# Kernel optimization log

Hardware: AMD Instinct MI355X
Metric: run time of the kernel (lower is better)

Reference implementation:

```python
import jax, jax.numpy as jnp
import numpy as np

B, S, D, H, HD = 1, 4096, 1024, 16, 64
HALF = HD // 2


def setup_inputs() -> dict:
    key = jax.random.key(0)
    ks = jax.random.split(key, 8)
    std = 0.02
    x = jax.random.normal(ks[0], (B, S, D), dtype=jnp.float32)
    wq_w = jax.random.normal(ks[1], (D, D), dtype=jnp.float32) * std
    wk_w = jax.random.normal(ks[2], (D, D), dtype=jnp.float32) * std
    wv_w = jax.random.normal(ks[3], (D, D), dtype=jnp.float32) * std
    wo_w = jax.random.normal(ks[4], (D, D), dtype=jnp.float32) * std
    wq_b = jnp.zeros((D,), jnp.float32)
    wk_b = jnp.zeros((D,), jnp.float32)
    wv_b = jnp.zeros((D,), jnp.float32)
    wo_b = jnp.zeros((D,), jnp.float32)
    # LLaMA-style rotary frequencies: theta = 10000^{-2i/HD}
    inv_freq = 1.0 / (10000.0 ** (jnp.arange(0, HD, 2, dtype=jnp.float32) / HD))  # [HALF]
    t = jnp.arange(S, dtype=jnp.float32)
    angles = jnp.outer(t, inv_freq)  # [S, HALF]
    freqs_cos = jnp.cos(angles)
    freqs_sin = jnp.sin(angles)
    # causal additive mask (finite large-negative to stay grad-safe)
    mask = jnp.triu(jnp.full((S, S), -1e9, dtype=jnp.float32), k=1)[None, None]
    return {
        "x": x, "start_pos": 0, "freqs_cos": freqs_cos, "freqs_sin": freqs_sin,
        "mask": mask,
        "wq_w": wq_w, "wq_b": wq_b, "wk_w": wk_w, "wk_b": wk_b,
        "wv_w": wv_w, "wv_b": wv_b, "wo_w": wo_w, "wo_b": wo_b,
    }


def _apply_rope(t, cos, sin):
    # t: [B, S, H, HD]; cos/sin: [S, HALF]. Complex multiply on consecutive pairs.
    b, s, h, hd = t.shape
    t2 = t.reshape(b, s, h, hd // 2, 2)
    x0, x1 = t2[..., 0], t2[..., 1]
    c = cos[None, :, None, :]
    sn = sin[None, :, None, :]
    o0 = x0 * c - x1 * sn
    o1 = x0 * sn + x1 * c
    return jnp.stack([o0, o1], axis=-1).reshape(b, s, h, hd)


def reference(x, start_pos, freqs_cos, freqs_sin, mask,
              wq_w, wq_b, wk_w, wk_b, wv_w, wv_b, wo_w, wo_b):
    bsz, seqlen, dim = x.shape
    q = (x @ wq_w.T + wq_b).reshape(bsz, seqlen, H, HD)
    k = (x @ wk_w.T + wk_b).reshape(bsz, seqlen, H, HD)
    v = (x @ wv_w.T + wv_b).reshape(bsz, seqlen, H, HD)
    q = _apply_rope(q, freqs_cos, freqs_sin)
    k = _apply_rope(k, freqs_cos, freqs_sin)
    # [B, H, S, HD]
    q = q.transpose(0, 2, 1, 3)
    k = k.transpose(0, 2, 1, 3)
    v = v.transpose(0, 2, 1, 3)
    scores = jnp.einsum('bhqd,bhkd->bhqk', q, k) / jnp.sqrt(jnp.float32(HD))
    scores = scores + mask
    probs = jax.nn.softmax(scores.astype(jnp.float32), axis=-1).astype(q.dtype)
    out = jnp.einsum('bhqk,bhkd->bhqd', probs, v)  # [B, H, S, HD]
    out = out.transpose(0, 2, 1, 3).reshape(bsz, seqlen, dim)
    return out @ wo_w.T + wo_b
```

## Files before the change

kernel.cpp:

```cpp
#include <hip/hip_runtime.h>


#define S_LEN 4096
#define DIM   1024
#define NH    16
#define HD    64

typedef __attribute__((ext_vector_type(8))) short bf16x8;
typedef __attribute__((ext_vector_type(4))) float f32x4;

__device__ __forceinline__ unsigned short f2b(float f) {
  union { float f; unsigned int u; } v; v.f = f;
  unsigned int r = (v.u + 0x7fffu + ((v.u >> 16) & 1u)) >> 16;
  return (unsigned short)r;
}
__device__ __forceinline__ float b2f(unsigned short h) {
  union { unsigned int u; float f; } v; v.u = ((unsigned int)h) << 16;
  return v.f;
}
__device__ __forceinline__ unsigned int pk2t(float a, float b) {
  union { float f; unsigned int u; } x, y; x.f = a; y.f = b;
  return (x.u >> 16) | (y.u & 0xffff0000u);
}
__device__ __forceinline__ void gload16(const void* g, void* l) {
  __builtin_amdgcn_global_load_lds(
      (const __attribute__((address_space(1))) unsigned int*)g,
      (__attribute__((address_space(3))) unsigned int*)l, 16, 0, 0);
}
__device__ __forceinline__ f32x4 fzero4() { f32x4 z = {0.f, 0.f, 0.f, 0.f}; return z; }

__device__ __forceinline__ bf16x8 lds_swz(const unsigned short* s, int row, int chunk) {
  int byte = row * 128 + ((chunk ^ (row & 7)) << 4);
  return *(const bf16x8*)((const char*)s + byte);
}

__global__ void cvt_all(const float* __restrict__ x, const float* __restrict__ wq,
                        const float* __restrict__ wk, const float* __restrict__ wv,
                        const float* __restrict__ wo, const float* __restrict__ qb,
                        const float* __restrict__ kb, const float* __restrict__ vbs,
                        const float* __restrict__ ob, unsigned short* __restrict__ xb,
                        unsigned short* __restrict__ wqkvb, unsigned short* __restrict__ wobb,
                        float* __restrict__ biasq, float* __restrict__ biaso) {
  int i = blockIdx.x * 256 + threadIdx.x;
  if (i < 2097152) {
    const float* src; unsigned short* dst; int off;
    if (i < 1048576)      { src = x;  dst = xb;              off = i; }
    else if (i < 1310720) { src = wq; dst = wqkvb;           off = i - 1048576; }
    else if (i < 1572864) { src = wk; dst = wqkvb + 1048576; off = i - 1310720; }
    else if (i < 1835008) { src = wv; dst = wqkvb + 2097152; off = i - 1572864; }
    else                  { src = wo; dst = wobb;            off = i - 1835008; }
    float4 v = ((const float4*)src)[off];
    unsigned int lo = (unsigned int)f2b(v.x) | ((unsigned int)f2b(v.y) << 16);
    unsigned int hi = (unsigned int)f2b(v.z) | ((unsigned int)f2b(v.w) << 16);
    ((uint2*)dst)[off] = make_uint2(lo, hi);
  } else if (i < 2097152 + 1024) {
    int j = i - 2097152;
    if (j < 256)      ((float4*)biasq)[j]              = ((const float4*)qb)[j];
    else if (j < 512) ((float4*)(biasq + 1024))[j-256] = ((const float4*)kb)[j-256];
    else if (j < 768) ((float4*)(biasq + 2048))[j-512] = ((const float4*)vbs)[j-512];
    else              ((float4*)biaso)[j-768]          = ((const float4*)ob)[j-768];
  }
}

__global__ __launch_bounds__(512, 2) void gemm_qkv(
    const unsigned short* __restrict__ A, const unsigned short* __restrict__ B,
    const float* __restrict__ bias, unsigned short* __restrict__ dq,
    unsigned short* __restrict__ dk, unsigned short* __restrict__ vtout,
    const float* __restrict__ fc, const float* __restrict__ fs, int K) {
  __shared__ alignas(16) unsigned short sA[2][256 * 64];
  __shared__ alignas(16) unsigned short sB[2][256 * 64];
  const int tid = threadIdx.x;
  const int lane = tid & 63, wave = tid >> 6;
  const int ln = lane & 15, quad = lane >> 4;
  const int bm = blockIdx.x * 256, bn = blockIdx.y * 256;
  const int wr = (wave >> 2) * 128, wc = (wave & 3) * 64;
  const int NT = K >> 6;

  f32x4 acc[8][4];
#pragma unroll
  for (int i = 0; i < 8; ++i)
#pragma unroll
    for (int j = 0; j < 4; ++j) acc[i][j] = fzero4();

#define STAGE(tt, ch) do {                                                   \
    int o_ = ((ch) * 512 + tid) * 8;                                         \
    int row_ = o_ >> 6, c_ = (o_ >> 3) & 7;                                  \
    int col_ = ((tt) << 6) + ((c_ ^ (row_ & 7)) << 3);                       \
    int bs_ = (tt) & 1;                                                      \
    gload16(A + (size_t)(bm + row_) * K + col_, (char*)sA[bs_] + o_ * 2);    \
    gload16(B + (size_t)(bn + row_) * K + col_, (char*)sB[bs_] + o_ * 2);    \
  } while (0)
#define BAR()   __builtin_amdgcn_s_barrier()
#define LGKM0() asm volatile("s_waitcnt lgkmcnt(0)" ::: "memory")

  STAGE(0, 0); STAGE(0, 1); STAGE(0, 2); STAGE(0, 3); STAGE(1, 0);
  asm volatile("s_waitcnt vmcnt(2)" ::: "memory");
  BAR();

#pragma unroll 2
  for (int t = 0; t < 16; ++t) {
    const unsigned short* cA = sA[t & 1];
    const unsigned short* cB = sB[t & 1];
    bf16x8 a0[4], a1[4], b0[4], b1[4];

#pragma unroll
    for (int j = 0; j < 4; ++j) b0[j] = lds_swz(cB, wc + j * 16 + ln, quad);
#pragma unroll
    for (int i = 0; i < 4; ++i) a0[i] = lds_swz(cA, wr + i * 16 + ln, quad);
    if (t + 1 < NT) STAGE(t + 1, 1);
    BAR(); LGKM0();
    __builtin_amdgcn_s_setprio(1);
#pragma unroll
    for (int i = 0; i < 4; ++i)
#pragma unroll
      for (int j = 0; j < 4; ++j)
        acc[i][j] = __builtin_amdgcn_mfma_f32_16x16x32_bf16(a0[i], b0[j], acc[i][j], 0, 0, 0);
    __builtin_amdgcn_s_setprio(0);
    BAR();

#pragma unroll
    for (int i = 0; i < 4; ++i) a1[i] = lds_swz(cA, wr + (i + 4) * 16 + ln, quad);
#pragma unroll
    for (int j = 0; j < 4; ++j) b1[j] = lds_swz(cB, wc + j * 16 + ln, 4 + quad);
    if (t + 1 < NT) STAGE(t + 1, 2);
    BAR(); LGKM0();
    __builtin_amdgcn_s_setprio(1);
#pragma unroll
    for (int i = 0; i < 4; ++i)
#pragma unroll
      for (int j = 0; j < 4; ++j)
        acc[i + 4][j] = __builtin_amdgcn_mfma_f32_16x16x32_bf16(a1[i], b0[j], acc[i + 4][j], 0, 0, 0);
    __builtin_amdgcn_s_setprio(0);
    BAR();

#pragma unroll
    for (int i = 0; i < 4; ++i) a0[i] = lds_swz(cA, wr + i * 16 + ln, 4 + quad);
#pragma unroll
    for (int i = 0; i < 4; ++i) a1[i] = lds_swz(cA, wr + (i + 4) * 16 + ln, 4 + quad);
    if (t + 1 < NT) STAGE(t + 1, 3);
    BAR(); LGKM0();
    __builtin_amdgcn_s_setprio(1);
#pragma unroll
    for (int i = 0; i < 4; ++i)
#pragma unroll
      for (int j = 0; j < 4; ++j)
        acc[i][j] = __builtin_amdgcn_mfma_f32_16x16x32_bf16(a0[i], b1[j], acc[i][j], 0, 0, 0);
    __builtin_amdgcn_s_setprio(0);
    BAR();

    if (t + 2 < NT) STAGE(t + 2, 0);
    BAR(); LGKM0();
    __builtin_amdgcn_s_setprio(1);
#pragma unroll
    for (int i = 0; i < 4; ++i)
#pragma unroll
      for (int j = 0; j < 4; ++j)
        acc[i + 4][j] = __builtin_amdgcn_mfma_f32_16x16x32_bf16(a1[i], b1[j], acc[i + 4][j], 0, 0, 0);
    __builtin_amdgcn_s_setprio(0);
    if (t < 14) {
      asm volatile("s_waitcnt vmcnt(2)" ::: "memory");
      BAR();
    } else if (t == 14) {
      asm volatile("s_waitcnt vmcnt(0)" ::: "memory");
      BAR();
    }
  }
#undef STAGE
#undef BAR
#undef LGKM0

  const int bufi = bn >> 10;
  const int hq = ((bn & 1023) + wc) >> 6;
  if (bufi < 2) {
    unsigned short* const base = bufi == 0 ? dq : dk;
    const float qsc = bufi == 0 ? 0.180336880f : 1.0f;
#pragma unroll
    for (int i = 0; i < 8; ++i)
#pragma unroll
      for (int j = 0; j < 4; ++j) {
        int n = bn + wc + j * 16 + ln;
        float bi = bias[n];
        int hd = j * 16 + ln;
        int pi = hd >> 1;
        bool evn = (ln & 1) == 0;
#pragma unroll
        for (int r = 0; r < 4; ++r) {
          int m = bm + wr + i * 16 + quad * 4 + r;
          float val = acc[i][j][r] + bi;
          float par = __shfl_xor(val, 1);
          float c = fc[m * 32 + pi], sn = fs[m * 32 + pi];
          float o = evn ? (val * c - par * sn) : (par * sn + val * c);
          base[((size_t)(hq * S_LEN + m)) * HD + hd] = f2b(o * qsc);
        }
      }
  } else {
    __syncthreads();
    unsigned short* scr =
        (wave < 4 ? (unsigned short*)sA : (unsigned short*)sB) + (wave & 3) * 8192;
#pragma unroll
    for (int i = 0; i < 8; ++i)
#pragma unroll
      for (int j = 0; j < 4; ++j) {
        int n = bn + wc + j * 16 + ln;
        float bi = bias[n];
        int hd = j * 16 + ln;
#pragma unroll
        for (int r = 0; r < 4; ++r) {
          int sl = i * 16 + quad * 4 + r;
          int byte = hd * 256 + ((((sl >> 3) ^ (hd & 7)) << 4)) + (sl & 7) * 2;
          *(unsigned short*)((char*)scr + byte) = f2b(acc[i][j][r] + bi);
        }
      }
    __syncthreads();
#pragma unroll
    for (int pass = 0; pass < 4; ++pass) {
      int row = pass * 16 + ln;
      uint4 d[4];
#pragma unroll
      for (int j = 0; j < 4; ++j) {
        int c = quad * 4 + j;
        d[j] = *(uint4*)((char*)scr + row * 256 + ((c ^ (row & 7)) << 4));
      }
      uint4* dst = (uint4*)(vtout + ((size_t)(hq * HD + row)) * S_LEN + bm + wr + quad * 32);
#pragma unroll
      for (int j = 0; j < 4; ++j) dst[j] = d[j];
    }
  }
}

__global__ __launch_bounds__(256) void gemm_out(
    const unsigned short* __restrict__ A, const unsigned short* __restrict__ B,
    const float* __restrict__ bias, float* __restrict__ outF, int N, int K) {
  __shared__ alignas(16) unsigned short sA[2][128 * 32];
  __shared__ alignas(16) unsigned short sB[2][64 * 32];
  const int tid = threadIdx.x;
  const int lane = tid & 63, wave = tid >> 6;
  const int ln = lane & 15, quad = lane >> 4;
  const int bm = blockIdx.x * 128, bn = blockIdx.y * 64;
  const int wr = (wave >> 1) * 64, wc = (wave & 1) * 32;

  f32x4 acc[4][2];
#pragma unroll
  for (int i = 0; i < 4; ++i)
#pragma unroll
    for (int j = 0; j < 2; ++j) acc[i][j] = fzero4();

  {
#pragma unroll
    for (int i = 0; i < 2; ++i) {
      int o = (i * 256 + tid) * 16;
      int e = o >> 1;
      int row = e >> 5, col = e & 31;
      gload16(A + (size_t)(bm + row) * K + col, (char*)sA[0] + o);
    }
    int o = tid * 16;
    int e = o >> 1;
    int row = e >> 5, col = e & 31;
    gload16(B + (size_t)(bn + row) * K + col, (char*)sB[0] + o);
  }

  int buf = 0;
  for (int k0 = 0; k0 < K; k0 += 32, buf ^= 1) {
    __syncthreads();
    if (k0 + 32 < K) {
#pragma unroll
      for (int i = 0; i < 2; ++i) {
        int o = (i * 256 + tid) * 16;
        int e = o >> 1;
        int row = e >> 5, col = e & 31;
        gload16(A + (size_t)(bm + row) * K + k0 + 32 + col, (char*)sA[buf ^ 1] + o);
      }
      int o = tid * 16;
      int e = o >> 1;
      int row = e >> 5, col = e & 31;
      gload16(B + (size_t)(bn + row) * K + k0 + 32 + col, (char*)sB[buf ^ 1] + o);
    }
    bf16x8 af[4], bfr[2];
#pragma unroll
    for (int i = 0; i < 4; ++i)
      af[i] = *(const bf16x8*)&sA[buf][(wr + i * 16 + ln) * 32 + quad * 8];
#pragma unroll
    for (int j = 0; j < 2; ++j)
      bfr[j] = *(const bf16x8*)&sB[buf][(wc + j * 16 + ln) * 32 + quad * 8];
#pragma unroll
    for (int i = 0; i < 4; ++i)
#pragma unroll
      for (int j = 0; j < 2; ++j)
        acc[i][j] = __builtin_amdgcn_mfma_f32_16x16x32_bf16(af[i], bfr[j], acc[i][j], 0, 0, 0);
  }

#pragma unroll
  for (int i = 0; i < 4; ++i)
#pragma unroll
    for (int j = 0; j < 2; ++j) {
      int n = bn + wc + j * 16 + ln;
      float bi = bias[n];
#pragma unroll
      for (int r = 0; r < 4; ++r) {
        int m = bm + wr + i * 16 + quad * 4 + r;
        outF[(size_t)m * N + n] = acc[i][j][r] + bi;
      }
    }
}

__global__ __launch_bounds__(512, 4) void flash_kernel(
    const unsigned short* __restrict__ qg, const unsigned short* __restrict__ kg,
    const unsigned short* __restrict__ vtg, unsigned short* __restrict__ attn) {
  __shared__ alignas(16) unsigned short sK[2][2][64 * 64];
  __shared__ alignas(16) unsigned short sV[2][2][64 * 64];

  const int tid = threadIdx.x;
  const int lane = tid & 63, wave = tid >> 6;
  const int w = wave & 3, grp = wave >> 2;
  const int ln = lane & 15, quad = lane >> 4;
  const int c = blockIdx.x;
  const int h = c & 15;
  const int qt = 63 - (c >> 4);
  const int qrow = qt * 64 + w * 16;

  const unsigned short* qh = qg + (size_t)h * (S_LEN * HD);
  const unsigned short* kh = kg + (size_t)h * (S_LEN * HD);
  const unsigned short* vh = vtg + (size_t)h * (HD * S_LEN);

  bf16x8 qf[2];
  qf[0] = *(const bf16x8*)(qh + (size_t)(qrow + ln) * HD + quad * 8);
  qf[1] = *(const bf16x8*)(qh + (size_t)(qrow + ln) * HD + 32 + quad * 8);

  f32x4 o_acc[4];
  f32x4 l_acc = fzero4();
#pragma unroll
  for (int t = 0; t < 4; ++t) o_acc[t] = fzero4();
  bf16x8 ones;
#pragma unroll
  for (int j = 0; j < 8; ++j) ones[j] = (short)0x3F80;

  const int nst = (qt + 2) >> 1;
  const int srow = tid >> 3, sch = tid & 7;
  const int kswz = (sch ^ (srow & 7)) << 3;

  gload16(kh + (size_t)srow * HD + kswz, (char*)sK[0][0] + tid * 16);
  gload16(kh + (size_t)(64 + srow) * HD + kswz, (char*)sK[0][1] + tid * 16);
  gload16(vh + (size_t)srow * S_LEN + kswz, (char*)sV[0][0] + tid * 16);
  gload16(vh + (size_t)srow * S_LEN + 64 + kswz, (char*)sV[0][1] + tid * 16);

  const unsigned short* kEp = kh + (size_t)(128 + srow) * HD + kswz;
  const unsigned short* kOp = kEp + (size_t)64 * HD;
  const unsigned short* vEp = vh + (size_t)srow * S_LEN + 128 + kswz;
  const unsigned short* vOp = vEp + 64;

  int buf = 0;
  for (int s = 0; s < nst; ++s, buf ^= 1) {
    __syncthreads();
    if (s + 1 < nst) {
      gload16(kEp, (char*)sK[buf ^ 1][0] + tid * 16);
      gload16(kOp, (char*)sK[buf ^ 1][1] + tid * 16);
      gload16(vEp, (char*)sV[buf ^ 1][0] + tid * 16);
      gload16(vOp, (char*)sV[buf ^ 1][1] + tid * 16);
      kEp += (size_t)128 * HD; kOp += (size_t)128 * HD;
      vEp += 128; vOp += 128;
    }
    const int kt = 2 * s + grp;
    if (kt > qt) continue;
    const unsigned short* kp = sK[buf][grp];
    const unsigned short* vp = sV[buf][grp];

    f32x4 sc[4];
#pragma unroll
    for (int t = 0; t < 4; ++t) sc[t] = fzero4();
    __builtin_amdgcn_s_setprio(1);
#pragma unroll
    for (int t = 0; t < 4; ++t) {
      bf16x8 kb0 = lds_swz(kp, t * 16 + ln, quad);
      bf16x8 kb1 = lds_swz(kp, t * 16 + ln, 4 + quad);
      sc[t] = __builtin_amdgcn_mfma_f32_16x16x32_bf16(kb0, qf[0], sc[t], 0, 0, 0);
      sc[t] = __builtin_amdgcn_mfma_f32_16x16x32_bf16(kb1, qf[1], sc[t], 0, 0, 0);
    }
    __builtin_amdgcn_s_setprio(0);

    float e[4][4];
    if (kt == qt) {
#pragma unroll
      for (int t = 0; t < 4; ++t)
#pragma unroll
        for (int r = 0; r < 4; ++r) {
          int kvl = 16 * t + quad * 4 + r;
          e[t][r] = (kvl <= w * 16 + ln) ? __builtin_amdgcn_exp2f(sc[t][r]) : 0.0f;
        }
    } else {
#pragma unroll
      for (int t = 0; t < 4; ++t)
#pragma unroll
        for (int r = 0; r < 4; ++r) e[t][r] = __builtin_amdgcn_exp2f(sc[t][r]);
    }

    unsigned int x0 = pk2t(e[0][0], e[0][1]), x1 = pk2t(e[0][2], e[0][3]);
    unsigned int y0 = pk2t(e[1][0], e[1][1]), y1 = pk2t(e[1][2], e[1][3]);
    unsigned int z0 = pk2t(e[2][0], e[2][1]), z1 = pk2t(e[2][2], e[2][3]);
    unsigned int w0 = pk2t(e[3][0], e[3][1]), w1 = pk2t(e[3][2], e[3][3]);
    auto a32 = __builtin_amdgcn_permlane32_swap(x0, y0, false, false);
    auto a16 = __builtin_amdgcn_permlane16_swap(a32[0], a32[1], false, false);
    auto b32 = __builtin_amdgcn_permlane32_swap(x1, y1, false, false);
    auto b16 = __builtin_amdgcn_permlane16_swap(b32[0], b32[1], false, false);
    auto c32 = __builtin_amdgcn_permlane32_swap(z0, w0, false, false);
    auto c16 = __builtin_amdgcn_permlane16_swap(c32[0], c32[1], false, false);
    auto d32 = __builtin_amdgcn_permlane32_swap(z1, w1, false, false);
    auto d16 = __builtin_amdgcn_permlane16_swap(d32[0], d32[1], false, false);
    union { uint4 u; bf16x8 b; } pa0u, pa1u;
    pa0u.u = make_uint4(a16[0], b16[0], a16[1], b16[1]);
    pa1u.u = make_uint4(c16[0], d16[0], c16[1], d16[1]);
    const bf16x8 pa0 = pa0u.b, pa1 = pa1u.b;

    __builtin_amdgcn_s_setprio(1);
    l_acc = __builtin_amdgcn_mfma_f32_16x16x32_bf16(pa0, ones, l_acc, 0, 0, 0);
    l_acc = __builtin_amdgcn_mfma_f32_16x16x32_bf16(pa1, ones, l_acc, 0, 0, 0);
#pragma unroll
    for (int t = 0; t < 4; ++t) {
      bf16x8 vb0 = lds_swz(vp, t * 16 + ln, quad);
      bf16x8 vb1 = lds_swz(vp, t * 16 + ln, 4 + quad);
      o_acc[t] = __builtin_amdgcn_mfma_f32_16x16x32_bf16(pa0, vb0, o_acc[t], 0, 0, 0);
      o_acc[t] = __builtin_amdgcn_mfma_f32_16x16x32_bf16(pa1, vb1, o_acc[t], 0, 0, 0);
    }
    __builtin_amdgcn_s_setprio(0);
  }

  __syncthreads();
  float* mrg = (float*)sK;
  const int mi = (w * 64 + lane) * 20;
  if (grp == 1) {
    *(f32x4*)&mrg[mi +  0] = o_acc[0];
    *(f32x4*)&mrg[mi +  4] = o_acc[1];
    *(f32x4*)&mrg[mi +  8] = o_acc[2];
    *(f32x4*)&mrg[mi + 12] = o_acc[3];
    *(f32x4*)&mrg[mi + 16] = l_acc;
  }
  __syncthreads();
  if (grp == 0) {
    o_acc[0] += *(const f32x4*)&mrg[mi + 0];
    o_acc[1] += *(const f32x4*)&mrg[mi + 4];
    o_acc[2] += *(const f32x4*)&mrg[mi + 8];
    o_acc[3] += *(const f32x4*)&mrg[mi + 12];
    l_acc += *(const f32x4*)&mrg[mi + 16];
    float inv[4];
#pragma unroll
    for (int r = 0; r < 4; ++r) inv[r] = 1.0f / l_acc[r];
#pragma unroll
    for (int t = 0; t < 4; ++t)
#pragma unroll
      for (int r = 0; r < 4; ++r) {
        int row = qrow + quad * 4 + r;
        attn[(size_t)row * DIM + h * HD + t * 16 + ln] = f2b(o_acc[t][r] * inv[r]);
      }
  }
}

extern "C" void kernel_launch(void* const* d_in, const int* in_sizes, int n_in,
                              void* d_out, int out_size, void* d_ws, size_t ws_size,
                              hipStream_t stream) {
  const float* x    = (const float*)d_in[0];
  const float* fc   = (const float*)d_in[2];
  const float* fs   = (const float*)d_in[3];
  const float* wqw  = (const float*)d_in[5];
  const float* wqb  = (const float*)d_in[6];
  const float* wkw  = (const float*)d_in[7];
  const float* wkb  = (const float*)d_in[8];
  const float* wvw  = (const float*)d_in[9];
  const float* wvb  = (const float*)d_in[10];
  const float* wow  = (const float*)d_in[11];
  const float* wobf = (const float*)d_in[12];
  float* out = (float*)d_out;

  char* ws = (char*)d_ws;
  const size_t MB = (size_t)1 << 20;
  unsigned short* xb    = (unsigned short*)(ws + 0);
  unsigned short* wqkvb = (unsigned short*)(ws + 8 * MB);
  unsigned short* wobb  = (unsigned short*)(ws + 16 * MB);
  float* biasq = (float*)(ws + 18 * MB);
  float* biaso = (float*)(ws + 18 * MB + 65536);
  unsigned short* qb_ = (unsigned short*)(ws + 19 * MB);
  unsigned short* kb_ = (unsigned short*)(ws + 27 * MB);
  unsigned short* vt  = (unsigned short*)(ws + 35 * MB);
  unsigned short* attn = (unsigned short*)(ws + 0);

  cvt_all<<<8196, 256, 0, stream>>>(x, wqw, wkw, wvw, wow, wqb, wkb, wvb, wobf,
                                    xb, wqkvb, wobb, biasq, biaso);
  gemm_qkv<<<dim3(16, 12), 512, 0, stream>>>(xb, wqkvb, biasq, qb_, kb_, vt, fc, fs, 1024);
  flash_kernel<<<1024, 512, 0, stream>>>(qb_, kb_, vt, attn);
  gemm_out<<<dim3(32, 16), 256, 0, stream>>>(attn, wobb, biaso, out, 1024, 1024);
}
```

Before: 247.7 us.

## Process 128-row query tiles per block so K/V tiles are reused twice

Each wave now handles 32 query rows (two 16-row fragments) instead of 16, so every block covers 128 query rows and the grid is halved. Each K and V fragment read from LDS feeds two MFMA chains, which halves LDS traffic and K/V global loads per query row. The query-tile order is also remapped to interleave long and short causal tiles for load balance. In exchange, each wave holds more registers, fewer blocks run, and the merge step uses both the K and V shared buffers.

```diff
diff --git a/kernel.cpp b/kernel.cpp
--- a/kernel.cpp
+++ b/kernel.cpp
@@ -315,26 +315,30 @@
   const int ln = lane & 15, quad = lane >> 4;
   const int c = blockIdx.x;
   const int h = c & 15;
-  const int qt = 63 - (c >> 4);
-  const int qrow = qt * 64 + w * 16;
+  const int k5 = c >> 4;
+  const int P = (k5 < 16) ? (31 - k5) : (k5 - 16);
+  const int qrow = P * 128 + w * 32;
+  const int nst = P + 1;
 
   const unsigned short* qh = qg + (size_t)h * (S_LEN * HD);
   const unsigned short* kh = kg + (size_t)h * (S_LEN * HD);
   const unsigned short* vh = vtg + (size_t)h * (HD * S_LEN);
 
-  bf16x8 qf[2];
-  qf[0] = *(const bf16x8*)(qh + (size_t)(qrow + ln) * HD + quad * 8);
-  qf[1] = *(const bf16x8*)(qh + (size_t)(qrow + ln) * HD + 32 + quad * 8);
-
-  f32x4 o_acc[4];
-  f32x4 l_acc = fzero4();
-#pragma unroll
-  for (int t = 0; t < 4; ++t) o_acc[t] = fzero4();
+  bf16x8 qf[2][2];
+#pragma unroll
+  for (int f = 0; f < 2; ++f) {
+    qf[f][0] = *(const bf16x8*)(qh + (size_t)(qrow + 16 * f + ln) * HD + quad * 8);
+    qf[f][1] = *(const bf16x8*)(qh + (size_t)(qrow + 16 * f + ln) * HD + 32 + quad * 8);
+  }
+
+  f32x4 o0[4], o1[4];
+  f32x4 l0 = fzero4(), l1 = fzero4();
+#pragma unroll
+  for (int t = 0; t < 4; ++t) { o0[t] = fzero4(); o1[t] = fzero4(); }
   bf16x8 ones;
 #pragma unroll
   for (int j = 0; j < 8; ++j) ones[j] = (short)0x3F80;
 
-  const int nst = (qt + 2) >> 1;
   const int srow = tid >> 3, sch = tid & 7;
   const int kswz = (sch ^ (srow & 7)) << 3;
 
@@ -360,95 +364,130 @@
       vEp += 128; vOp += 128;
     }
     const int kt = 2 * s + grp;
-    if (kt > qt) continue;
+    const int kv0 = kt * 64;
+    if (kv0 > qrow + 31) continue;
     const unsigned short* kp = sK[buf][grp];
     const unsigned short* vp = sV[buf][grp];
-
-    f32x4 sc[4];
-#pragma unroll
-    for (int t = 0; t < 4; ++t) sc[t] = fzero4();
-    __builtin_amdgcn_s_setprio(1);
-#pragma unroll
-    for (int t = 0; t < 4; ++t) {
-      bf16x8 kb0 = lds_swz(kp, t * 16 + ln, quad);
-      bf16x8 kb1 = lds_swz(kp, t * 16 + ln, 4 + quad);
-      sc[t] = __builtin_amdgcn_mfma_f32_16x16x32_bf16(kb0, qf[0], sc[t], 0, 0, 0);
-      sc[t] = __builtin_amdgcn_mfma_f32_16x16x32_bf16(kb1, qf[1], sc[t], 0, 0, 0);
-    }
-    __builtin_amdgcn_s_setprio(0);
-
-    float e[4][4];
-    if (kt == qt) {
-#pragma unroll
-      for (int t = 0; t < 4; ++t)
+    const int dq = qrow - kv0;
+    const bool m0 = (dq < 63), m1 = (dq + 16 < 63);
+
+#pragma unroll
+    for (int H = 0; H < 2; ++H) {
+      bf16x8 kA0 = lds_swz(kp, H * 32 + ln, quad);
+      bf16x8 kA1 = lds_swz(kp, H * 32 + ln, 4 + quad);
+      bf16x8 kB0 = lds_swz(kp, H * 32 + 16 + ln, quad);
+      bf16x8 kB1 = lds_swz(kp, H * 32 + 16 + ln, 4 + quad);
+      f32x4 sA0 = fzero4(), sB0 = fzero4(), sA1 = fzero4(), sB1 = fzero4();
+      __builtin_amdgcn_s_setprio(1);
+      sA0 = __builtin_amdgcn_mfma_f32_16x16x32_bf16(kA0, qf[0][0], sA0, 0, 0, 0);
+      sA0 = __builtin_amdgcn_mfma_f32_16x16x32_bf16(kA1, qf[0][1], sA0, 0, 0, 0);
+      sB0 = __builtin_amdgcn_mfma_f32_16x16x32_bf16(kB0, qf[0][0], sB0, 0, 0, 0);
+      sB0 = __builtin_amdgcn_mfma_f32_16x16x32_bf16(kB1, qf[0][1], sB0, 0, 0, 0);
+      sA1 = __builtin_amdgcn_mfma_f32_16x16x32_bf16(kA0, qf[1][0], sA1, 0, 0, 0);
+      sA1 = __builtin_amdgcn_mfma_f32_16x16x32_bf16(kA1, qf[1][1], sA1, 0, 0, 0);
+      sB1 = __builtin_amdgcn_mfma_f32_16x16x32_bf16(kB0, qf[1][0], sB1, 0, 0, 0);
+      sB1 = __builtin_amdgcn_mfma_f32_16x16x32_bf16(kB1, qf[1][1], sB1, 0, 0, 0);
+      __builtin_amdgcn_s_setprio(0);
+
+      const int ka = H * 32 + 4 * quad;
+      const int kbv = ka + 16;
+      float eA0[4], eB0[4], eA1[4], eB1[4];
+      if (m0) {
 #pragma unroll
         for (int r = 0; r < 4; ++r) {
-          int kvl = 16 * t + quad * 4 + r;
-          e[t][r] = (kvl <= w * 16 + ln) ? __builtin_amdgcn_exp2f(sc[t][r]) : 0.0f;
+          eA0[r] = (ka + r <= dq + ln) ? __builtin_amdgcn_exp2f(sA0[r]) : 0.0f;
+          eB0[r] = (kbv + r <= dq + ln) ? __builtin_amdgcn_exp2f(sB0[r]) : 0.0f;
         }
-    } else {
-#pragma unroll
-      for (int t = 0; t < 4; ++t)
-#pragma unroll
-        for (int r = 0; r < 4; ++r) e[t][r] = __builtin_amdgcn_exp2f(sc[t][r]);
-    }
-
-    unsigned int x0 = pk2t(e[0][0], e[0][1]), x1 = pk2t(e[0][2], e[0][3]);
-    unsigned int y0 = pk2t(e[1][0], e[1][1]), y1 = pk2t(e[1][2], e[1][3]);
-    unsigned int z0 = pk2t(e[2][0], e[2][1]), z1 = pk2t(e[2][2], e[2][3]);
-    unsigned int w0 = pk2t(e[3][0], e[3][1]), w1 = pk2t(e[3][2], e[3][3]);
-    auto a32 = __builtin_amdgcn_permlane32_swap(x0, y0, false, false);
-    auto a16 = __builtin_amdgcn_permlane16_swap(a32[0], a32[1], false, false);
-    auto b32 = __builtin_amdgcn_permlane32_swap(x1, y1, false, false);
-    auto b16 = __builtin_amdgcn_permlane16_swap(b32[0], b32[1], false, false);
-    auto c32 = __builtin_amdgcn_permlane32_swap(z0, w0, false, false);
-    auto c16 = __builtin_amdgcn_permlane16_swap(c32[0], c32[1], false, false);
-    auto d32 = __builtin_amdgcn_permlane32_swap(z1, w1, false, false);
-    auto d16 = __builtin_amdgcn_permlane16_swap(d32[0], d32[1], false, false);
-    union { uint4 u; bf16x8 b; } pa0u, pa1u;
-    pa0u.u = make_uint4(a16[0], b16[0], a16[1], b16[1]);
-    pa1u.u = make_uint4(c16[0], d16[0], c16[1], d16[1]);
-    const bf16x8 pa0 = pa0u.b, pa1 = pa1u.b;
-
-    __builtin_amdgcn_s_setprio(1);
-    l_acc = __builtin_amdgcn_mfma_f32_16x16x32_bf16(pa0, ones, l_acc, 0, 0, 0);
-    l_acc = __builtin_amdgcn_mfma_f32_16x16x32_bf16(pa1, ones, l_acc, 0, 0, 0);
-#pragma unroll
-    for (int t = 0; t < 4; ++t) {
-      bf16x8 vb0 = lds_swz(vp, t * 16 + ln, quad);
-      bf16x8 vb1 = lds_swz(vp, t * 16 + ln, 4 + quad);
-      o_acc[t] = __builtin_amdgcn_mfma_f32_16x16x32_bf16(pa0, vb0, o_acc[t], 0, 0, 0);
-      o_acc[t] = __builtin_amdgcn_mfma_f32_16x16x32_bf16(pa1, vb1, o_acc[t], 0, 0, 0);
-    }
-    __builtin_amdgcn_s_setprio(0);
+      } else {
+#pragma unroll
+        for (int r = 0; r < 4; ++r) {
+          eA0[r] = __builtin_amdgcn_exp2f(sA0[r]);
+          eB0[r] = __builtin_amdgcn_exp2f(sB0[r]);
+        }
+      }
+      if (m1) {
+#pragma unroll
+        for (int r = 0; r < 4; ++r) {
+          eA1[r] = (ka + r <= dq + 16 + ln) ? __builtin_amdgcn_exp2f(sA1[r]) : 0.0f;
+          eB1[r] = (kbv + r <= dq + 16 + ln) ? __builtin_amdgcn_exp2f(sB1[r]) : 0.0f;
+        }
+      } else {
+#pragma unroll
+        for (int r = 0; r < 4; ++r) {
+          eA1[r] = __builtin_amdgcn_exp2f(sA1[r]);
+          eB1[r] = __builtin_amdgcn_exp2f(sB1[r]);
+        }
+      }
+
+      unsigned int x0 = pk2t(eA0[0], eA0[1]), x1 = pk2t(eA0[2], eA0[3]);
+      unsigned int y0 = pk2t(eB0[0], eB0[1]), y1 = pk2t(eB0[2], eB0[3]);
+      auto a32 = __builtin_amdgcn_permlane32_swap(x0, y0, false, false);
+      auto a16 = __builtin_amdgcn_permlane16_swap(a32[0], a32[1], false, false);
+      auto b32 = __builtin_amdgcn_permlane32_swap(x1, y1, false, false);
+      auto b16 = __builtin_amdgcn_permlane16_swap(b32[0], b32[1], false, false);
+      union { uint4 u; bf16x8 b; } p0u, p1u;
+      p0u.u = make_uint4(a16[0], b16[0], a16[1], b16[1]);
+      unsigned int z0 = pk2t(eA1[0], eA1[1]), z1 = pk2t(eA1[2], eA1[3]);
+      unsigned int w0 = pk2t(eB1[0], eB1[1]), w1 = pk2t(eB1[2], eB1[3]);
+      auto c32 = __builtin_amdgcn_permlane32_swap(z0, w0, false, false);
+      auto c16 = __builtin_amdgcn_permlane16_swap(c32[0], c32[1], false, false);
+      auto d32 = __builtin_amdgcn_permlane32_swap(z1, w1, false, false);
+      auto d16 = __builtin_amdgcn_permlane16_swap(d32[0], d32[1], false, false);
+      p1u.u = make_uint4(c16[0], d16[0], c16[1], d16[1]);
+      const bf16x8 pa0 = p0u.b, pa1 = p1u.b;
+
+      __builtin_amdgcn_s_setprio(1);
+      l0 = __builtin_amdgcn_mfma_f32_16x16x32_bf16(pa0, ones, l0, 0, 0, 0);
+      l1 = __builtin_amdgcn_mfma_f32_16x16x32_bf16(pa1, ones, l1, 0, 0, 0);
+#pragma unroll
+      for (int t = 0; t < 4; ++t) {
+        bf16x8 vb = lds_swz(vp, t * 16 + ln, H * 4 + quad);
+        o0[t] = __builtin_amdgcn_mfma_f32_16x16x32_bf16(pa0, vb, o0[t], 0, 0, 0);
+        o1[t] = __builtin_amdgcn_mfma_f32_16x16x32_bf16(pa1, vb, o1[t], 0, 0, 0);
+      }
+      __builtin_amdgcn_s_setprio(0);
+    }
   }
 
   __syncthreads();
-  float* mrg = (float*)sK;
+  float* mrgK = (float*)sK;
+  float* mrgV = (float*)sV;
   const int mi = (w * 64 + lane) * 20;
   if (grp == 1) {
-    *(f32x4*)&mrg[mi +  0] = o_acc[0];
-    *(f32x4*)&mrg[mi +  4] = o_acc[1];
-    *(f32x4*)&mrg[mi +  8] = o_acc[2];
-    *(f32x4*)&mrg[mi + 12] = o_acc[3];
-    *(f32x4*)&mrg[mi + 16] = l_acc;
+    *(f32x4*)&mrgK[mi +  0] = o0[0];
+    *(f32x4*)&mrgK[mi +  4] = o0[1];
+    *(f32x4*)&mrgK[mi +  8] = o0[2];
+    *(f32x4*)&mrgK[mi + 12] = o0[3];
+    *(f32x4*)&mrgK[mi + 16] = l0;
+    *(f32x4*)&mrgV[mi +  0] = o1[0];
+    *(f32x4*)&mrgV[mi +  4] = o1[1];
+    *(f32x4*)&mrgV[mi +  8] = o1[2];
+    *(f32x4*)&mrgV[mi + 12] = o1[3];
+    *(f32x4*)&mrgV[mi + 16] = l1;
   }
   __syncthreads();
   if (grp == 0) {
-    o_acc[0] += *(const f32x4*)&mrg[mi + 0];
-    o_acc[1] += *(const f32x4*)&mrg[mi + 4];
-    o_acc[2] += *(const f32x4*)&mrg[mi + 8];
-    o_acc[3] += *(const f32x4*)&mrg[mi + 12];
-    l_acc += *(const f32x4*)&mrg[mi + 16];
-    float inv[4];
-#pragma unroll
-    for (int r = 0; r < 4; ++r) inv[r] = 1.0f / l_acc[r];
+    o0[0] += *(const f32x4*)&mrgK[mi + 0];
+    o0[1] += *(const f32x4*)&mrgK[mi + 4];
+    o0[2] += *(const f32x4*)&mrgK[mi + 8];
+    o0[3] += *(const f32x4*)&mrgK[mi + 12];
+    l0 += *(const f32x4*)&mrgK[mi + 16];
+    o1[0] += *(const f32x4*)&mrgV[mi + 0];
+    o1[1] += *(const f32x4*)&mrgV[mi + 4];
+    o1[2] += *(const f32x4*)&mrgV[mi + 8];
+    o1[3] += *(const f32x4*)&mrgV[mi + 12];
+    l1 += *(const f32x4*)&mrgV[mi + 16];
+    float i0[4], i1[4];
+#pragma unroll
+    for (int r = 0; r < 4; ++r) { i0[r] = 1.0f / l0[r]; i1[r] = 1.0f / l1[r]; }
 #pragma unroll
     for (int t = 0; t < 4; ++t)
 #pragma unroll
       for (int r = 0; r < 4; ++r) {
-        int row = qrow + quad * 4 + r;
-        attn[(size_t)row * DIM + h * HD + t * 16 + ln] = f2b(o_acc[t][r] * inv[r]);
+        int row0 = qrow + quad * 4 + r;
+        int row1 = qrow + 16 + quad * 4 + r;
+        attn[(size_t)row0 * DIM + h * HD + t * 16 + ln] = f2b(o0[t][r] * i0[r]);
+        attn[(size_t)row1 * DIM + h * HD + t * 16 + ln] = f2b(o1[t][r] * i1[r]);
       }
   }
 }
@@ -484,6 +523,6 @@
   cvt_all<<<8196, 256, 0, stream>>>(x, wqw, wkw, wvw, wow, wqb, wkb, wvb, wobf,
                                     xb, wqkvb, wobb, biasq, biaso);
   gemm_qkv<<<dim3(16, 12), 512, 0, stream>>>(xb, wqkvb, biasq, qb_, kb_, vt, fc, fs, 1024);
-  flash_kernel<<<1024, 512, 0, stream>>>(qb_, kb_, vt, attn);
+  flash_kernel<<<512, 512, 0, stream>>>(qb_, kb_, vt, attn);
   gemm_out<<<dim3(32, 16), 256, 0, stream>>>(attn, wobb, biaso, out, 1024, 1024);
 }
```

New measurement: 253.5 us. 1.02x slower.

## Load V fragments directly from global memory and convert P with hardware bf16 pack

Applied to the files above, without the earlier changes.

V tiles are no longer staged through double-buffered LDS. Each lane reads its transposed-V fragments straight from global memory into registers right before the PV MFMAs. This frees LDS, so launch bounds are raised to allow more resident blocks, and the merge buffer moves to its own dedicated shared array. The truncating bf16 pack of the exponentials is replaced with the hardware v_cvt_pk_bf16_f32 instruction, which rounds and slightly changes numerics. The risk is exposed global-load latency on the critical MFMA path, plus higher register pressure under the tighter occupancy bound.

```diff
diff --git a/kernel.cpp b/kernel.cpp
--- a/kernel.cpp
+++ b/kernel.cpp
@@ -21,6 +21,11 @@
 __device__ __forceinline__ unsigned int pk2t(float a, float b) {
   union { float f; unsigned int u; } x, y; x.f = a; y.f = b;
   return (x.u >> 16) | (y.u & 0xffff0000u);
+}
+__device__ __forceinline__ unsigned int cvtpk(float a, float b) {
+  unsigned int r;
+  asm("v_cvt_pk_bf16_f32 %0, %1, %2" : "=v"(r) : "v"(a), "v"(b));
+  return r;
 }
 __device__ __forceinline__ void gload16(const void* g, void* l) {
   __builtin_amdgcn_global_load_lds(
@@ -303,11 +308,11 @@
     }
 }
 
-__global__ __launch_bounds__(512, 4) void flash_kernel(
+__global__ __launch_bounds__(512, 6) void flash_kernel(
     const unsigned short* __restrict__ qg, const unsigned short* __restrict__ kg,
     const unsigned short* __restrict__ vtg, unsigned short* __restrict__ attn) {
   __shared__ alignas(16) unsigned short sK[2][2][64 * 64];
-  __shared__ alignas(16) unsigned short sV[2][2][64 * 64];
+  __shared__ alignas(16) float sMrg[5120];
 
   const int tid = threadIdx.x;
   const int lane = tid & 63, wave = tid >> 6;
@@ -338,15 +343,16 @@
   const int srow = tid >> 3, sch = tid & 7;
   const int kswz = (sch ^ (srow & 7)) << 3;
 
+  const unsigned short* vr[4];
+#pragma unroll
+  for (int t = 0; t < 4; ++t)
+    vr[t] = vh + (size_t)(t * 16 + ln) * S_LEN + quad * 8 + grp * 64;
+
   gload16(kh + (size_t)srow * HD + kswz, (char*)sK[0][0] + tid * 16);
   gload16(kh + (size_t)(64 + srow) * HD + kswz, (char*)sK[0][1] + tid * 16);
-  gload16(vh + (size_t)srow * S_LEN + kswz, (char*)sV[0][0] + tid * 16);
-  gload16(vh + (size_t)srow * S_LEN + 64 + kswz, (char*)sV[0][1] + tid * 16);
 
   const unsigned short* kEp = kh + (size_t)(128 + srow) * HD + kswz;
   const unsigned short* kOp = kEp + (size_t)64 * HD;
-  const unsigned short* vEp = vh + (size_t)srow * S_LEN + 128 + kswz;
-  const unsigned short* vOp = vEp + 64;
 
   int buf = 0;
   for (int s = 0; s < nst; ++s, buf ^= 1) {
@@ -354,15 +360,11 @@
     if (s + 1 < nst) {
       gload16(kEp, (char*)sK[buf ^ 1][0] + tid * 16);
       gload16(kOp, (char*)sK[buf ^ 1][1] + tid * 16);
-      gload16(vEp, (char*)sV[buf ^ 1][0] + tid * 16);
-      gload16(vOp, (char*)sV[buf ^ 1][1] + tid * 16);
       kEp += (size_t)128 * HD; kOp += (size_t)128 * HD;
-      vEp += 128; vOp += 128;
     }
     const int kt = 2 * s + grp;
     if (kt > qt) continue;
     const unsigned short* kp = sK[buf][grp];
-    const unsigned short* vp = sV[buf][grp];
 
     f32x4 sc[4];
 #pragma unroll
@@ -393,10 +395,10 @@
         for (int r = 0; r < 4; ++r) e[t][r] = __builtin_amdgcn_exp2f(sc[t][r]);
     }
 
-    unsigned int x0 = pk2t(e[0][0], e[0][1]), x1 = pk2t(e[0][2], e[0][3]);
-    unsigned int y0 = pk2t(e[1][0], e[1][1]), y1 = pk2t(e[1][2], e[1][3]);
-    unsigned int z0 = pk2t(e[2][0], e[2][1]), z1 = pk2t(e[2][2], e[2][3]);
-    unsigned int w0 = pk2t(e[3][0], e[3][1]), w1 = pk2t(e[3][2], e[3][3]);
+    unsigned int x0 = cvtpk(e[0][0], e[0][1]), x1 = cvtpk(e[0][2], e[0][3]);
+    unsigned int y0 = cvtpk(e[1][0], e[1][1]), y1 = cvtpk(e[1][2], e[1][3]);
+    unsigned int z0 = cvtpk(e[2][0], e[2][1]), z1 = cvtpk(e[2][2], e[2][3]);
+    unsigned int w0 = cvtpk(e[3][0], e[3][1]), w1 = cvtpk(e[3][2], e[3][3]);
     auto a32 = __builtin_amdgcn_permlane32_swap(x0, y0, false, false);
     auto a16 = __builtin_amdgcn_permlane16_swap(a32[0], a32[1], false, false);
     auto b32 = __builtin_amdgcn_permlane32_swap(x1, y1, false, false);
@@ -415,31 +417,31 @@
     l_acc = __builtin_amdgcn_mfma_f32_16x16x32_bf16(pa1, ones, l_acc, 0, 0, 0);
 #pragma unroll
     for (int t = 0; t < 4; ++t) {
-      bf16x8 vb0 = lds_swz(vp, t * 16 + ln, quad);
-      bf16x8 vb1 = lds_swz(vp, t * 16 + ln, 4 + quad);
+      bf16x8 vb0 = *(const bf16x8*)vr[t];
+      bf16x8 vb1 = *(const bf16x8*)(vr[t] + 32);
       o_acc[t] = __builtin_amdgcn_mfma_f32_16x16x32_bf16(pa0, vb0, o_acc[t], 0, 0, 0);
       o_acc[t] = __builtin_amdgcn_mfma_f32_16x16x32_bf16(pa1, vb1, o_acc[t], 0, 0, 0);
+      vr[t] += 128;
     }
     __builtin_amdgcn_s_setprio(0);
   }
 
   __syncthreads();
-  float* mrg = (float*)sK;
   const int mi = (w * 64 + lane) * 20;
   if (grp == 1) {
-    *(f32x4*)&mrg[mi +  0] = o_acc[0];
-    *(f32x4*)&mrg[mi +  4] = o_acc[1];
-    *(f32x4*)&mrg[mi +  8] = o_acc[2];
-    *(f32x4*)&mrg[mi + 12] = o_acc[3];
-    *(f32x4*)&mrg[mi + 16] = l_acc;
+    *(f32x4*)&sMrg[mi +  0] = o_acc[0];
+    *(f32x4*)&sMrg[mi +  4] = o_acc[1];
+    *(f32x4*)&sMrg[mi +  8] = o_acc[2];
+    *(f32x4*)&sMrg[mi + 12] = o_acc[3];
+    *(f32x4*)&sMrg[mi + 16] = l_acc;
   }
   __syncthreads();
   if (grp == 0) {
-    o_acc[0] += *(const f32x4*)&mrg[mi + 0];
-    o_acc[1] += *(const f32x4*)&mrg[mi + 4];
-    o_acc[2] += *(const f32x4*)&mrg[mi + 8];
-    o_acc[3] += *(const f32x4*)&mrg[mi + 12];
-    l_acc += *(const f32x4*)&mrg[mi + 16];
+    o_acc[0] += *(const f32x4*)&sMrg[mi + 0];
+    o_acc[1] += *(const f32x4*)&sMrg[mi + 4];
+    o_acc[2] += *(const f32x4*)&sMrg[mi + 8];
+    o_acc[3] += *(const f32x4*)&sMrg[mi + 12];
+    l_acc += *(const f32x4*)&sMrg[mi + 16];
     float inv[4];
 #pragma unroll
     for (int r = 0; r < 4; ++r) inv[r] = 1.0f / l_acc[r];
```

New measurement: 346.5 us. +39.9%, slower.

## Single-buffer V tile, load it during QK^T, raise flash occupancy

Applied to the files above, without the earlier changes.

The V tile in LDS drops from double to single buffering, and its global loads are issued at the start of each step. They overlap with the QK^T and softmax work, and a second barrier with a partial vmcnt wait guards the PV stage. Launch bounds move from 4 to 6 blocks per CU so the smaller LDS footprint can allow more resident blocks. The cost is an extra barrier per iteration and less prefetch slack for V. The higher occupancy target may also raise register pressure.

```diff
diff --git a/kernel.cpp b/kernel.cpp
--- a/kernel.cpp
+++ b/kernel.cpp
@@ -303,11 +303,11 @@
     }
 }
 
-__global__ __launch_bounds__(512, 4) void flash_kernel(
+__global__ __launch_bounds__(512, 6) void flash_kernel(
     const unsigned short* __restrict__ qg, const unsigned short* __restrict__ kg,
     const unsigned short* __restrict__ vtg, unsigned short* __restrict__ attn) {
   __shared__ alignas(16) unsigned short sK[2][2][64 * 64];
-  __shared__ alignas(16) unsigned short sV[2][2][64 * 64];
+  __shared__ alignas(16) unsigned short sV[2][64 * 64];
 
   const int tid = threadIdx.x;
   const int lane = tid & 63, wave = tid >> 6;
@@ -340,87 +340,97 @@
 
   gload16(kh + (size_t)srow * HD + kswz, (char*)sK[0][0] + tid * 16);
   gload16(kh + (size_t)(64 + srow) * HD + kswz, (char*)sK[0][1] + tid * 16);
-  gload16(vh + (size_t)srow * S_LEN + kswz, (char*)sV[0][0] + tid * 16);
-  gload16(vh + (size_t)srow * S_LEN + 64 + kswz, (char*)sV[0][1] + tid * 16);
-
+
+  const unsigned short* vEp = vh + (size_t)srow * S_LEN + kswz;
+  const unsigned short* vOp = vEp + 64;
   const unsigned short* kEp = kh + (size_t)(128 + srow) * HD + kswz;
   const unsigned short* kOp = kEp + (size_t)64 * HD;
-  const unsigned short* vEp = vh + (size_t)srow * S_LEN + 128 + kswz;
-  const unsigned short* vOp = vEp + 64;
 
   int buf = 0;
   for (int s = 0; s < nst; ++s, buf ^= 1) {
-    __syncthreads();
-    if (s + 1 < nst) {
+    asm volatile("s_waitcnt vmcnt(0)" ::: "memory");
+    __builtin_amdgcn_s_barrier();
+
+    gload16(vEp, (char*)sV[0] + tid * 16);
+    gload16(vOp, (char*)sV[1] + tid * 16);
+    vEp += 128; vOp += 128;
+    const bool pk = (s + 1 < nst);
+    if (pk) {
       gload16(kEp, (char*)sK[buf ^ 1][0] + tid * 16);
       gload16(kOp, (char*)sK[buf ^ 1][1] + tid * 16);
-      gload16(vEp, (char*)sV[buf ^ 1][0] + tid * 16);
-      gload16(vOp, (char*)sV[buf ^ 1][1] + tid * 16);
       kEp += (size_t)128 * HD; kOp += (size_t)128 * HD;
-      vEp += 128; vOp += 128;
-    }
+    }
+
     const int kt = 2 * s + grp;
-    if (kt > qt) continue;
-    const unsigned short* kp = sK[buf][grp];
-    const unsigned short* vp = sV[buf][grp];
-
-    f32x4 sc[4];
-#pragma unroll
-    for (int t = 0; t < 4; ++t) sc[t] = fzero4();
-    __builtin_amdgcn_s_setprio(1);
-#pragma unroll
-    for (int t = 0; t < 4; ++t) {
-      bf16x8 kb0 = lds_swz(kp, t * 16 + ln, quad);
-      bf16x8 kb1 = lds_swz(kp, t * 16 + ln, 4 + quad);
-      sc[t] = __builtin_amdgcn_mfma_f32_16x16x32_bf16(kb0, qf[0], sc[t], 0, 0, 0);
-      sc[t] = __builtin_amdgcn_mfma_f32_16x16x32_bf16(kb1, qf[1], sc[t], 0, 0, 0);
-    }
-    __builtin_amdgcn_s_setprio(0);
-
-    float e[4][4];
-    if (kt == qt) {
-#pragma unroll
-      for (int t = 0; t < 4; ++t)
-#pragma unroll
-        for (int r = 0; r < 4; ++r) {
-          int kvl = 16 * t + quad * 4 + r;
-          e[t][r] = (kvl <= w * 16 + ln) ? __builtin_amdgcn_exp2f(sc[t][r]) : 0.0f;
-        }
-    } else {
-#pragma unroll
-      for (int t = 0; t < 4; ++t)
-#pragma unroll
-        for (int r = 0; r < 4; ++r) e[t][r] = __builtin_amdgcn_exp2f(sc[t][r]);
-    }
-
-    unsigned int x0 = pk2t(e[0][0], e[0][1]), x1 = pk2t(e[0][2], e[0][3]);
-    unsigned int y0 = pk2t(e[1][0], e[1][1]), y1 = pk2t(e[1][2], e[1][3]);
-    unsigned int z0 = pk2t(e[2][0], e[2][1]), z1 = pk2t(e[2][2], e[2][3]);
-    unsigned int w0 = pk2t(e[3][0], e[3][1]), w1 = pk2t(e[3][2], e[3][3]);
-    auto a32 = __builtin_amdgcn_permlane32_swap(x0, y0, false, false);
-    auto a16 = __builtin_amdgcn_permlane16_swap(a32[0], a32[1], false, false);
-    auto b32 = __builtin_amdgcn_permlane32_swap(x1, y1, false, false);
-    auto b16 = __builtin_amdgcn_permlane16_swap(b32[0], b32[1], false, false);
-    auto c32 = __builtin_amdgcn_permlane32_swap(z0, w0, false, false);
-    auto c16 = __builtin_amdgcn_permlane16_swap(c32[0], c32[1], false, false);
-    auto d32 = __builtin_amdgcn_permlane32_swap(z1, w1, false, false);
-    auto d16 = __builtin_amdgcn_permlane16_swap(d32[0], d32[1], false, false);
-    union { uint4 u; bf16x8 b; } pa0u, pa1u;
-    pa0u.u = make_uint4(a16[0], b16[0], a16[1], b16[1]);
-    pa1u.u = make_uint4(c16[0], d16[0], c16[1], d16[1]);
-    const bf16x8 pa0 = pa0u.b, pa1 = pa1u.b;
-
-    __builtin_amdgcn_s_setprio(1);
-    l_acc = __builtin_amdgcn_mfma_f32_16x16x32_bf16(pa0, ones, l_acc, 0, 0, 0);
-    l_acc = __builtin_amdgcn_mfma_f32_16x16x32_bf16(pa1, ones, l_acc, 0, 0, 0);
-#pragma unroll
-    for (int t = 0; t < 4; ++t) {
-      bf16x8 vb0 = lds_swz(vp, t * 16 + ln, quad);
-      bf16x8 vb1 = lds_swz(vp, t * 16 + ln, 4 + quad);
-      o_acc[t] = __builtin_amdgcn_mfma_f32_16x16x32_bf16(pa0, vb0, o_acc[t], 0, 0, 0);
-      o_acc[t] = __builtin_amdgcn_mfma_f32_16x16x32_bf16(pa1, vb1, o_acc[t], 0, 0, 0);
-    }
-    __builtin_amdgcn_s_setprio(0);
+    const bool act = (kt <= qt);
+    bf16x8 pa0, pa1;
+    if (act) {
+      const unsigned short* kp = sK[buf][grp];
+      f32x4 sc[4];
+#pragma unroll
+      for (int t = 0; t < 4; ++t) sc[t] = fzero4();
+      __builtin_amdgcn_s_setprio(1);
+#pragma unroll
+      for (int t = 0; t < 4; ++t) {
+        bf16x8 kb0 = lds_swz(kp, t * 16 + ln, quad);
+        bf16x8 kb1 = lds_swz(kp, t * 16 + ln, 4 + quad);
+        sc[t] = __builtin_amdgcn_mfma_f32_16x16x32_bf16(kb0, qf[0], sc[t], 0, 0, 0);
+        sc[t] = __builtin_amdgcn_mfma_f32_16x16x32_bf16(kb1, qf[1], sc[t], 0, 0, 0);
+      }
+      __builtin_amdgcn_s_setprio(0);
+
+      float e[4][4];
+      if (kt == qt) {
+#pragma unroll
+        for (int t = 0; t < 4; ++t)
+#pragma unroll
+          for (int r = 0; r < 4; ++r) {
+            int kvl = 16 * t + quad * 4 + r;
+            e[t][r] = (kvl <= w * 16 + ln) ? __builtin_amdgcn_exp2f(sc[t][r]) : 0.0f;
+          }
+      } else {
+#pragma unroll
+        for (int t = 0; t < 4; ++t)
+#pragma unroll
+          for (int r = 0; r < 4; ++r) e[t][r] = __builtin_amdgcn_exp2f(sc[t][r]);
+      }
+
+      unsigned int x0 = pk2t(e[0][0], e[0][1]), x1 = pk2t(e[0][2], e[0][3]);
+      unsigned int y0 = pk2t(e[1][0], e[1][1]), y1 = pk2t(e[1][2], e[1][3]);
+      unsigned int z0 = pk2t(e[2][0], e[2][1]), z1 = pk2t(e[2][2], e[2][3]);
+      unsigned int w0 = pk2t(e[3][0], e[3][1]), w1 = pk2t(e[3][2], e[3][3]);
+      auto a32 = __builtin_amdgcn_permlane32_swap(x0, y0, false, false);
+      auto a16 = __builtin_amdgcn_permlane16_swap(a32[0], a32[1], false, false);
+      auto b32 = __builtin_amdgcn_permlane32_swap(x1, y1, false, false);
+      auto b16 = __builtin_amdgcn_permlane16_swap(b32[0], b32[1], false, false);
+      auto c32 = __builtin_amdgcn_permlane32_swap(z0, w0, false, false);
+      auto c16 = __builtin_amdgcn_permlane16_swap(c32[0], c32[1], false, false);
+      auto d32 = __builtin_amdgcn_permlane32_swap(z1, w1, false, false);
+      auto d16 = __builtin_amdgcn_permlane16_swap(d32[0], d32[1], false, false);
+      union { uint4 u; bf16x8 b; } pa0u, pa1u;
+      pa0u.u = make_uint4(a16[0], b16[0], a16[1], b16[1]);
+      pa1u.u = make_uint4(c16[0], d16[0], c16[1], d16[1]);
+      pa0 = pa0u.b; pa1 = pa1u.b;
+    }
+
+    if (pk) asm volatile("s_waitcnt vmcnt(2)" ::: "memory");
+    else    asm volatile("s_waitcnt vmcnt(0)" ::: "memory");
+    __builtin_amdgcn_s_barrier();
+
+    if (act) {
+      const unsigned short* vp = sV[grp];
+      __builtin_amdgcn_s_setprio(1);
+      l_acc = __builtin_amdgcn_mfma_f32_16x16x32_bf16(pa0, ones, l_acc, 0, 0, 0);
+      l_acc = __builtin_amdgcn_mfma_f32_16x16x32_bf16(pa1, ones, l_acc, 0, 0, 0);
+#pragma unroll
+      for (int t = 0; t < 4; ++t) {
+        bf16x8 vb0 = lds_swz(vp, t * 16 + ln, quad);
+        bf16x8 vb1 = lds_swz(vp, t * 16 + ln, 4 + quad);
+        o_acc[t] = __builtin_amdgcn_mfma_f32_16x16x32_bf16(pa0, vb0, o_acc[t], 0, 0, 0);
+        o_acc[t] = __builtin_amdgcn_mfma_f32_16x16x32_bf16(pa1, vb1, o_acc[t], 0, 0, 0);
+      }
+      __builtin_amdgcn_s_setprio(0);
+    }
   }
 
   __syncthreads();
```

New measurement: 245.0 us. No clear change (-1.1%).
